# Kernel optimization log

Hardware: AMD Instinct MI355X
Metric: run time of the kernel (lower is better)

## Reference

```python
import jax, jax.numpy as jnp
import numpy as np

EPS = 1e-6
INF = 1e30  # stands in for 'no value' in the sparse C_bar lists of the torch code


def setup_inputs() -> dict:
    key = jax.random.key(0)
    M, N, D = 512, 256, 64
    kx, ky, kq = jax.random.split(key, 3)
    x = jax.random.normal(kx, (M, D), dtype=jnp.float32)
    y = jax.random.normal(ky, (N, D), dtype=jnp.float32)
    u = jax.random.uniform(kq, (N + 1, N), dtype=jnp.float32, minval=0.05, maxval=1.0)
    q = u / jnp.sum(u, axis=0, keepdims=True)  # column-stochastic jump probabilities
    return {"x": x, "y": y, "q": q}


def _pal_forward(x, y, q):
    M, N = x.shape[0], y.shape[0]
    dt = x.dtype

    # ---- compute_dists: pairwise L2 (p=2 norm), M x N ----
    diff = x[:, None, :] - y[None, :, :]
    dists = jnp.sqrt(jnp.sum(diff * diff, axis=2))

    # ---- compute_reachability: sequential accumulation over columns of q ----
    def reach_step(p, nb):
        return p + p[nb] * q[:, nb], None
    p0 = jnp.zeros(N + 1, dtype=dt).at[0].set(1.0)
    p, _ = jax.lax.scan(reach_step, p0, jnp.arange(N))
    p_back = p[:N][None, :] * q / (p[:, None] + EPS)  # (N+1, N)

    # ---- edge structure: ancestors n_bar < n with p_back > 0 (detached mask) ----
    tri = jnp.tril(jnp.ones((N, N), dtype=bool), k=-1)
    E = tri & (jax.lax.stop_gradient(p_back[:N]) > 0)   # (N, N): E[n, n_bar]
    w = jnp.where(E, p_back[:N], 0.0)                   # mixing weights

    ns = jnp.arange(1, N)

    def row_dp(d_row, base0, C_prev, Cbar_prev):
        """One row m of the lattice. C_prev: C[m-1] (N,), Cbar_prev: C_bar[m-1] (N,N).
        Returns C[m] (N,) and C_bar[m] (N,N) with INF at non-edge slots."""
        C0 = jnp.zeros(N, dtype=dt).at[0].set(d_row[0] + base0)

        def n_step(Ccur, n):
            # min over: C[m][n_bar] (insert y), C[m-1][n_bar] (match), C_bar[m-1][n][n_bar] (insert x)
            c_min = jnp.minimum(Ccur, jnp.minimum(C_prev, Cbar_prev[n]))  # (N,) over n_bar
            cbar = d_row[n] + c_min
            val = jnp.sum(jnp.where(E[n], w[n] * cbar, 0.0))
            return Ccur.at[n].set(val), jnp.where(E[n], cbar, INF)

        C_row, Cbar_rows = jax.lax.scan(n_step, C0, ns)
        Cbar = jnp.concatenate([jnp.full((1, N), INF, dt), Cbar_rows], axis=0)
        return C_row, Cbar

    # m = 0: no previous row -> previous-row candidates disabled via INF, C[0][0] = d[0,0]
    C_row0, Cbar0 = row_dp(dists[0], jnp.zeros((), dt), jnp.full(N, INF, dt), jnp.full((N, N), INF, dt))

    def m_step(carry, d_row):
        C_prev, Cbar_prev = carry
        C_row, Cbar = row_dp(d_row, C_prev[0], C_prev, Cbar_prev)  # C[m][0] = d[m,0] + C[m-1][0]
        return (C_row, Cbar), None

    (C_last, _), _ = jax.lax.scan(m_step, (C_row0, Cbar0), dists[1:])

    # expected cost of reaching END from each terminal n
    return jnp.sum(p_back[N] * C_last)


def reference(x, y, q):
    return _pal_forward(x, y, q)
```

## Files before the change

### kernel.cpp

```cpp
#include <hip/hip_runtime.h>

typedef float f4 __attribute__((ext_vector_type(4)));

#define Nn 256
#define Mm 512
#define Dd 64
#define EPSF 1e-6f
#define INFF 1e30f
#define BC 8
#define NCHUNK (Nn / BC)
#define R 16
#define NBLK 8
#define CW 4
#define SST (NBLK * CW)
#define SLOTS 4

#define OFF_D     0
#define OFF_QC    131072
#define OFF_P     (OFF_QC + 65792)
#define OFF_WT    (OFF_P + 260)
#define OFF_WS    (OFF_WT + 65536)
#define OFF_CBAR  (OFF_WS + 256)
#define OFF_CROW  (OFF_CBAR + 65536)
#define OFF_FLAG  (OFF_CROW + SST*Nn)

__device__ __forceinline__ int llc_load_int(const int* p) {
  int v;
  asm volatile("global_load_dword %0, %1, off sc0 sc1\n\ts_waitcnt vmcnt(0)"
               : "=v"(v) : "v"(p) : "memory");
  return v;
}
__device__ __forceinline__ void llc_store_int(int* p, int v) {
  asm volatile("global_store_dword %0, %1, off sc0 sc1" :: "v"(p), "v"(v) : "memory");
}
__device__ __forceinline__ void llc_load_cbar10(const float* b0, const float* cp,
                                                f4 c[8], f4& pl, f4& ph) {
  const float* b1 = b0 + 4 * Nn;
  asm volatile(
    "global_load_dwordx4 %0, %10, off sc0 sc1\n\t"
    "global_load_dwordx4 %1, %10, off offset:1024 sc0 sc1\n\t"
    "global_load_dwordx4 %2, %10, off offset:2048 sc0 sc1\n\t"
    "global_load_dwordx4 %3, %10, off offset:3072 sc0 sc1\n\t"
    "global_load_dwordx4 %4, %11, off sc0 sc1\n\t"
    "global_load_dwordx4 %5, %11, off offset:1024 sc0 sc1\n\t"
    "global_load_dwordx4 %6, %11, off offset:2048 sc0 sc1\n\t"
    "global_load_dwordx4 %7, %11, off offset:3072 sc0 sc1\n\t"
    "global_load_dwordx4 %8, %12, off sc0 sc1\n\t"
    "global_load_dwordx4 %9, %12, off offset:16 sc0 sc1\n\t"
    "s_waitcnt vmcnt(0)"
    : "=v"(c[0]), "=v"(c[1]), "=v"(c[2]), "=v"(c[3]),
      "=v"(c[4]), "=v"(c[5]), "=v"(c[6]), "=v"(c[7]),
      "=v"(pl), "=v"(ph)
    : "v"(b0), "v"(b1), "v"(cp)
    : "memory");
}
__device__ __forceinline__ void llc_store_cbar8(float* b0, const f4 c[8]) {
  float* b1 = b0 + 4 * Nn;
  asm volatile(
    "global_store_dwordx4 %8, %0, off sc0 sc1\n\t"
    "global_store_dwordx4 %8, %1, off offset:1024 sc0 sc1\n\t"
    "global_store_dwordx4 %8, %2, off offset:2048 sc0 sc1\n\t"
    "global_store_dwordx4 %8, %3, off offset:3072 sc0 sc1\n\t"
    "global_store_dwordx4 %9, %4, off sc0 sc1\n\t"
    "global_store_dwordx4 %9, %5, off offset:1024 sc0 sc1\n\t"
    "global_store_dwordx4 %9, %6, off offset:2048 sc0 sc1\n\t"
    "global_store_dwordx4 %9, %7, off offset:3072 sc0 sc1\n\t"
    "s_waitcnt vmcnt(0)"
    :: "v"(c[0]), "v"(c[1]), "v"(c[2]), "v"(c[3]),
       "v"(c[4]), "v"(c[5]), "v"(c[6]), "v"(c[7]),
       "v"(b0), "v"(b1)
    : "memory");
}
__device__ __forceinline__ float rdlane(float v, int l) {
  return __int_as_float(__builtin_amdgcn_readlane(__float_as_int(v), l));
}

__global__ __launch_bounds__(256) void k_pre(const float* __restrict__ x,
                                             const float* __restrict__ y,
                                             const float* __restrict__ q,
                                             float* __restrict__ ws) {
  const int b = blockIdx.x, t = threadIdx.x;
  if (b < Mm) {
    __shared__ float xs[Dd];
    if (t < Dd) xs[t] = x[b * Dd + t];
    __syncthreads();
    const float4* y4 = (const float4*)(y + t * Dd);
    float acc = 0.f;
#pragma unroll
    for (int k = 0; k < Dd / 4; k++) {
      float4 v = y4[k];
      float a0 = xs[4*k+0] - v.x, a1 = xs[4*k+1] - v.y;
      float a2 = xs[4*k+2] - v.z, a3 = xs[4*k+3] - v.w;
      acc += a0*a0 + a1*a1 + a2*a2 + a3*a3;
    }
    ws[OFF_D + b * Nn + t] = sqrtf(acc);
  } else if (b < Mm + 257) {
    const int j = b - Mm;
    ws[OFF_QC + t * 257 + j] = q[j * Nn + t];
  } else {
    ws[OFF_WS + t] = 0.f;
    if (t < NBLK * NCHUNK) ((int*)(ws + OFF_FLAG))[t] = 0;
  }
}

__global__ __launch_bounds__(256) void k_reach(const float* __restrict__ qc, float* __restrict__ p_out) {
  __shared__ float p[257];
  __shared__ float vsnap[64];
  __shared__ float qtile[64][65];
  int tid = threadIdx.x;
  p[tid] = (tid == 0) ? 1.f : 0.f;
  if (tid == 0) p[256] = 0.f;
  __syncthreads();
  for (int g = 0; g < 4; g++) {
    int g0 = g * 64;
    for (int z = 0; z < 16; z++) {
      int idx = tid + z * 256, k = idx >> 6, l = idx & 63;
      qtile[k][l] = qc[(g0 + k) * 257 + g0 + l];
    }
    __syncthreads();
    if (tid < 64) {
      float pv = p[g0 + tid];
      for (int k = 0; k < 64; k++) {
        float v = __shfl(pv, k, 64);
        if (tid == k) vsnap[k] = v;
        pv += v * qtile[k][tid];
      }
    }
    __syncthreads();
    float acc = p[tid];
    float acc2 = (tid == 0) ? p[256] : 0.f;
    for (int k = 0; k < 64; k++) {
      float v = vsnap[k];
      acc += v * qc[(g0 + k) * 257 + tid];
      if (tid == 0) acc2 += v * qc[(g0 + k) * 257 + 256];
    }
    __syncthreads();
    p[tid] = acc;
    if (tid == 0) p[256] = acc2;
    __syncthreads();
  }
  p_out[tid] = p[tid];
  if (tid == 0) p_out[256] = p[256];
}

__global__ __launch_bounds__(256) void k_wbuild(const float* __restrict__ qc, const float* __restrict__ p,
                                                float* __restrict__ wT, float* __restrict__ Wsum) {
  int t = blockIdx.x, n = threadIdx.x;
  float v = 0.f;
  if (t < n) v = p[t] * qc[t * 257 + n] / (p[n] + EPSF);
  wT[t * Nn + n] = v;
  if (v != 0.f) atomicAdd(&Wsum[n], v);
}

__global__ __launch_bounds__(320, 1) void k_main(const float* __restrict__ d,
                                                 const float* __restrict__ wT,
                                                 const float* __restrict__ Wsum,
                                                 float* __restrict__ cbarG,
                                                 float* __restrict__ crowG,
                                                 int* __restrict__ flags,
                                                 const float* __restrict__ q,
                                                 const float* __restrict__ p,
                                                 float* __restrict__ out) {
  __shared__ __align__(16) float sbuf[SLOTS][BC * Nn];
  __shared__ __align__(16) float stg[2][BC * Nn];
  __shared__ __align__(16) float stg_cr[2][8];
  __shared__ __align__(16) float crow_lds[CW][SLOTS][BC];
  __shared__ __align__(16) float crow_fin[Nn];

  const int tid  = threadIdx.x;
  const int wave = tid >> 6;
  const int lane = tid & 63;
  const int blk  = blockIdx.x;
  const int stage = blk * CW + wave;
  const int m0 = stage * R;

  f4 dl[R], S[R], Wt;
  if (wave < CW) {
#pragma unroll
    for (int r = 0; r < R; r++) {
      dl[r] = *(const f4*)(d + (m0 + r) * Nn + 4 * lane);
      S[r] = (f4){0.f, 0.f, 0.f, 0.f};
    }
    Wt = *(const f4*)(Wsum + 4 * lane);
  }

  if (wave == CW && blk > 0) {
    const int* fp = flags + (blk - 1) * NCHUNK;
    while (llc_load_int(fp) == 0) __builtin_amdgcn_s_sleep(1);
    f4 c0[BC], pl, ph;
    llc_load_cbar10(cbarG + 4 * lane, crowG + (blk - 1) * Nn, c0, pl, ph);
#pragma unroll
    for (int tt = 0; tt < BC; tt++) *(f4*)&stg[0][tt * Nn + 4 * lane] = c0[tt];
    if (lane == 0) { *(f4*)&stg_cr[0][0] = pl; *(f4*)&stg_cr[0][4] = ph; }
  }
  __syncthreads();

#pragma clang loop unroll(disable)
  for (int s = 0; s < NCHUNK + CW - 1; s++) {
    if (wave < CW) {
      const int j = s - wave;
      if (j >= 0 && j < NCHUNK) {
        f4 wv[BC];
#pragma unroll
        for (int tt = 0; tt < BC; tt++)
          wv[tt] = *(const f4*)(wT + (j * BC + tt) * Nn + 4 * lane);

        f4 c[BC], cpl, cph;
        float* lsl = &sbuf[j & (SLOTS - 1)][0] + 4 * lane;

        if (wave == 0) {
          if (blk > 0) {
#pragma unroll
            for (int tt = 0; tt < BC; tt++) c[tt] = *(const f4*)&stg[j & 1][tt * Nn + 4 * lane];
            cpl = *(const f4*)&stg_cr[j & 1][0];
            cph = *(const f4*)&stg_cr[j & 1][4];
          } else {
            cpl = (f4){INFF, INFF, INFF, INFF};
            cph = cpl;
#pragma unroll
            for (int tt = 0; tt < BC; tt++) c[tt] = cpl;
          }
        } else {
#pragma unroll
          for (int tt = 0; tt < BC; tt++) c[tt] = *(const f4*)(lsl + tt * Nn);
          const float* cr = &crow_lds[wave - 1][j & (SLOTS - 1)][0];
          cpl = *(const f4*)cr;
          cph = *(const f4*)(cr + 4);
        }

        f4 clast4;
        const bool isJ0 = (j == 0);
#pragma unroll
        for (int tt = 0; tt < BC; tt++) {
          const int owner = 2 * j + (tt >> 2);
          const int comp = tt & 3;
          const bool isT0 = isJ0 && (tt == 0);

          float up = (tt < 4) ? cpl[comp] : cph[comp];
          float prcMin = up;
          float prcVal = up;
          if (isT0 && stage == 0) prcVal = 0.f;
          float cml[R];
#pragma unroll
          for (int r = 0; r < R; r++) {
            float Cv;
            if (isT0) Cv = dl[r][0] + prcVal;
            else      Cv = fmaf(dl[r][comp], Wt[comp], S[r][comp]);
            cml[r] = fminf(Cv, prcMin);
            prcVal = Cv;
            prcMin = Cv;
          }
          float cmB[R];
#pragma unroll
          for (int r = 0; r < R; r++) cmB[r] = rdlane(cml[r], owner);
          float clastv = rdlane(prcVal, owner);
          if (lane == owner) clast4[comp] = clastv;

#pragma unroll
          for (int k = 0; k < 4; k++) {
            float w_ = wv[tt][k];
            if (w_ > 0.f) {
              float cbv = c[tt][k];
#pragma unroll
              for (int r = 0; r < R; r++) {
                float a = fminf(cmB[r], cbv);
                S[r][k] = fmaf(w_, a, S[r][k]);
                cbv = dl[r][k] + a;
              }
              c[tt][k] = cbv;
            }
          }
        }

        if (wave < CW - 1) {
#pragma unroll
          for (int tt = 0; tt < BC; tt++) *(f4*)(lsl + tt * Nn) = c[tt];
          if (lane == 2 * j || lane == 2 * j + 1)
            *(f4*)&crow_lds[wave][j & (SLOTS - 1)][(lane & 1) * 4] = clast4;
        } else if (blk < NBLK - 1) {
          if (lane == 2 * j || lane == 2 * j + 1) {
            float* cp = crowG + blk * Nn + j * BC + (lane & 1) * 4;
            asm volatile("global_store_dwordx4 %0, %1, off sc0 sc1" :: "v"(cp), "v"(clast4) : "memory");
          }
          llc_store_cbar8(cbarG + (size_t)j * BC * Nn + 4 * lane, c);
          if (lane == 0) llc_store_int(flags + blk * NCHUNK + j, 1);
        } else {
          if (lane == 2 * j || lane == 2 * j + 1)
            *(f4*)&crow_fin[j * BC + (lane & 1) * 4] = clast4;
        }
      }
    } else {
      const int jn = s + 1;
      if (blk > 0 && jn < NCHUNK) {
        const int* fp = flags + (blk - 1) * NCHUNK + jn;
        while (llc_load_int(fp) == 0) __builtin_amdgcn_s_sleep(1);
        f4 cn[BC], pl, ph;
        llc_load_cbar10(cbarG + (size_t)jn * BC * Nn + 4 * lane,
                        crowG + (blk - 1) * Nn + jn * BC, cn, pl, ph);
#pragma unroll
        for (int tt = 0; tt < BC; tt++) *(f4*)&stg[jn & 1][tt * Nn + 4 * lane] = cn[tt];
        if (lane == 0) { *(f4*)&stg_cr[jn & 1][0] = pl; *(f4*)&stg_cr[jn & 1][4] = ph; }
      }
    }
    __syncthreads();
  }

  if (blk == NBLK - 1) {
    if (tid < Nn) {
      float fw = p[tid] * q[Nn * Nn + tid] / (p[Nn] + EPSF);
      crow_fin[tid] *= fw;
    }
    __syncthreads();
    for (int sft = 128; sft > 0; sft >>= 1) {
      if (tid < sft) crow_fin[tid] += crow_fin[tid + sft];
      __syncthreads();
    }
    if (tid == 0) out[0] = crow_fin[0];
  }
}

extern "C" void kernel_launch(void* const* d_in, const int* in_sizes, int n_in,
                              void* d_out, int out_size, void* d_ws, size_t ws_size,
                              hipStream_t stream) {
  const float* x = (const float*)d_in[0];
  const float* y = (const float*)d_in[1];
  const float* q = (const float*)d_in[2];
  float* ws = (float*)d_ws;
  float* out = (float*)d_out;
  hipLaunchKernelGGL(k_pre,   dim3(Mm + 257 + 1), dim3(256), 0, stream, x, y, q, ws);
  hipLaunchKernelGGL(k_reach, dim3(1),   dim3(256), 0, stream, ws + OFF_QC, ws + OFF_P);
  hipLaunchKernelGGL(k_wbuild,dim3(Nn),  dim3(256), 0, stream, ws + OFF_QC, ws + OFF_P,
                     ws + OFF_WT, ws + OFF_WS);
  hipLaunchKernelGGL(k_main,  dim3(NBLK), dim3(320), 0, stream, ws + OFF_D, ws + OFF_WT,
                     ws + OFF_WS, ws + OFF_CBAR, ws + OFF_CROW, (int*)(ws + OFF_FLAG),
                     q, ws + OFF_P, out);
}
```

Before: 493.9 us.

## Offload inter-block cbar stores and prefetch to dedicated waves

Adds two prefetch waves that poll predecessor flags ahead and fill an 8-slot staging ring, plus a store wave that drains LDS-staged outputs to global memory and publishes flags with a delay. The last compute wave now writes its chunk to LDS instead of performing blocking LLC stores and waits. This aims to take global-memory latency off the compute waves' critical path, at the cost of more threads, more LDS, and later flag publication to the next block.

```diff
diff --git a/kernel.cpp b/kernel.cpp
--- a/kernel.cpp
+++ b/kernel.cpp
@@ -12,8 +12,10 @@
 #define R 16
 #define NBLK 8
 #define CW 4
+#define NPF 2
 #define SST (NBLK * CW)
 #define SLOTS 4
+#define SSLOT 8
 
 #define OFF_D     0
 #define OFF_QC    131072
@@ -54,7 +56,7 @@
     : "v"(b0), "v"(b1), "v"(cp)
     : "memory");
 }
-__device__ __forceinline__ void llc_store_cbar8(float* b0, const f4 c[8]) {
+__device__ __forceinline__ void llc_store_cbar8_nw(float* b0, const f4 c[8]) {
   float* b1 = b0 + 4 * Nn;
   asm volatile(
     "global_store_dwordx4 %8, %0, off sc0 sc1\n\t"
@@ -64,8 +66,7 @@
     "global_store_dwordx4 %9, %4, off sc0 sc1\n\t"
     "global_store_dwordx4 %9, %5, off offset:1024 sc0 sc1\n\t"
     "global_store_dwordx4 %9, %6, off offset:2048 sc0 sc1\n\t"
-    "global_store_dwordx4 %9, %7, off offset:3072 sc0 sc1\n\t"
-    "s_waitcnt vmcnt(0)"
+    "global_store_dwordx4 %9, %7, off offset:3072 sc0 sc1"
     :: "v"(c[0]), "v"(c[1]), "v"(c[2]), "v"(c[3]),
        "v"(c[4]), "v"(c[5]), "v"(c[6]), "v"(c[7]),
        "v"(b0), "v"(b1)
@@ -152,7 +153,7 @@
   if (v != 0.f) atomicAdd(&Wsum[n], v);
 }
 
-__global__ __launch_bounds__(320, 1) void k_main(const float* __restrict__ d,
+__global__ __launch_bounds__(448, 1) void k_main(const float* __restrict__ d,
                                                  const float* __restrict__ wT,
                                                  const float* __restrict__ Wsum,
                                                  float* __restrict__ cbarG,
@@ -162,8 +163,10 @@
                                                  const float* __restrict__ p,
                                                  float* __restrict__ out) {
   __shared__ __align__(16) float sbuf[SLOTS][BC * Nn];
-  __shared__ __align__(16) float stg[2][BC * Nn];
-  __shared__ __align__(16) float stg_cr[2][8];
+  __shared__ __align__(16) float stg[SSLOT][BC * Nn];
+  __shared__ __align__(16) float stg_cr[SSLOT][8];
+  __shared__ __align__(16) float ostg[2][BC * Nn];
+  __shared__ __align__(16) float ostg_cr[2][8];
   __shared__ __align__(16) float crow_lds[CW][SLOTS][BC];
   __shared__ __align__(16) float crow_fin[Nn];
 
@@ -184,14 +187,21 @@
     Wt = *(const f4*)(Wsum + 4 * lane);
   }
 
-  if (wave == CW && blk > 0) {
-    const int* fp = flags + (blk - 1) * NCHUNK;
-    while (llc_load_int(fp) == 0) __builtin_amdgcn_s_sleep(1);
-    f4 c0[BC], pl, ph;
-    llc_load_cbar10(cbarG + 4 * lane, crowG + (blk - 1) * Nn, c0, pl, ph);
-#pragma unroll
-    for (int tt = 0; tt < BC; tt++) *(f4*)&stg[0][tt * Nn + 4 * lane] = c0[tt];
-    if (lane == 0) { *(f4*)&stg_cr[0][0] = pl; *(f4*)&stg_cr[0][4] = ph; }
+  int jn = NCHUNK, pend = 0;
+  if (wave >= CW && wave < CW + NPF) {
+    const int pf = wave - CW;
+    if (blk > 0) {
+      jn = pf;
+      const int* fp = flags + (blk - 1) * NCHUNK + jn;
+      while (llc_load_int(fp) == 0) __builtin_amdgcn_s_sleep(1);
+      f4 cn[BC], pl, ph;
+      llc_load_cbar10(cbarG + (size_t)jn * BC * Nn + 4 * lane,
+                      crowG + (blk - 1) * Nn + jn * BC, cn, pl, ph);
+#pragma unroll
+      for (int tt = 0; tt < BC; tt++) *(f4*)&stg[jn][tt * Nn + 4 * lane] = cn[tt];
+      if (lane == 0) { *(f4*)&stg_cr[jn][0] = pl; *(f4*)&stg_cr[jn][4] = ph; }
+      jn += NPF;
+    }
   }
   __syncthreads();
 
@@ -211,9 +221,9 @@
         if (wave == 0) {
           if (blk > 0) {
 #pragma unroll
-            for (int tt = 0; tt < BC; tt++) c[tt] = *(const f4*)&stg[j & 1][tt * Nn + 4 * lane];
-            cpl = *(const f4*)&stg_cr[j & 1][0];
-            cph = *(const f4*)&stg_cr[j & 1][4];
+            for (int tt = 0; tt < BC; tt++) c[tt] = *(const f4*)&stg[j & (SSLOT - 1)][tt * Nn + 4 * lane];
+            cpl = *(const f4*)&stg_cr[j & (SSLOT - 1)][0];
+            cph = *(const f4*)&stg_cr[j & (SSLOT - 1)][4];
           } else {
             cpl = (f4){INFF, INFF, INFF, INFF};
             cph = cpl;
@@ -278,31 +288,72 @@
           if (lane == 2 * j || lane == 2 * j + 1)
             *(f4*)&crow_lds[wave][j & (SLOTS - 1)][(lane & 1) * 4] = clast4;
         } else if (blk < NBLK - 1) {
-          if (lane == 2 * j || lane == 2 * j + 1) {
-            float* cp = crowG + blk * Nn + j * BC + (lane & 1) * 4;
-            asm volatile("global_store_dwordx4 %0, %1, off sc0 sc1" :: "v"(cp), "v"(clast4) : "memory");
-          }
-          llc_store_cbar8(cbarG + (size_t)j * BC * Nn + 4 * lane, c);
-          if (lane == 0) llc_store_int(flags + blk * NCHUNK + j, 1);
+#pragma unroll
+          for (int tt = 0; tt < BC; tt++) *(f4*)&ostg[j & 1][tt * Nn + 4 * lane] = c[tt];
+          if (lane == 2 * j || lane == 2 * j + 1)
+            *(f4*)&ostg_cr[j & 1][(lane & 1) * 4] = clast4;
         } else {
           if (lane == 2 * j || lane == 2 * j + 1)
             *(f4*)&crow_fin[j * BC + (lane & 1) * 4] = clast4;
         }
       }
+    } else if (wave < CW + NPF) {
+      if (blk > 0 && jn < NCHUNK) {
+        if (pend) {
+          f4 cn[BC], pl, ph;
+          llc_load_cbar10(cbarG + (size_t)jn * BC * Nn + 4 * lane,
+                          crowG + (blk - 1) * Nn + jn * BC, cn, pl, ph);
+#pragma unroll
+          for (int tt = 0; tt < BC; tt++) *(f4*)&stg[jn & (SSLOT - 1)][tt * Nn + 4 * lane] = cn[tt];
+          if (lane == 0) {
+            *(f4*)&stg_cr[jn & (SSLOT - 1)][0] = pl;
+            *(f4*)&stg_cr[jn & (SSLOT - 1)][4] = ph;
+          }
+          jn += NPF; pend = 0;
+        } else if (s >= jn - 4) {
+          const int* fp = flags + (blk - 1) * NCHUNK + jn;
+          if (s >= jn - 2) {
+            while (llc_load_int(fp) == 0) __builtin_amdgcn_s_sleep(1);
+            pend = 1;
+          } else if (llc_load_int(fp) != 0) pend = 1;
+        }
+      }
     } else {
-      const int jn = s + 1;
-      if (blk > 0 && jn < NCHUNK) {
-        const int* fp = flags + (blk - 1) * NCHUNK + jn;
-        while (llc_load_int(fp) == 0) __builtin_amdgcn_s_sleep(1);
-        f4 cn[BC], pl, ph;
-        llc_load_cbar10(cbarG + (size_t)jn * BC * Nn + 4 * lane,
-                        crowG + (blk - 1) * Nn + jn * BC, cn, pl, ph);
-#pragma unroll
-        for (int tt = 0; tt < BC; tt++) *(f4*)&stg[jn & 1][tt * Nn + 4 * lane] = cn[tt];
-        if (lane == 0) { *(f4*)&stg_cr[jn & 1][0] = pl; *(f4*)&stg_cr[jn & 1][4] = ph; }
+      if (blk < NBLK - 1) {
+        asm volatile("s_waitcnt vmcnt(0)" ::: "memory");
+        const int c_pub = s - 5;
+        if (c_pub >= 0 && lane == 0) llc_store_int(flags + blk * NCHUNK + c_pub, 1);
+        const int c_st = s - 4;
+        if (c_st >= 0 && c_st < NCHUNK) {
+          f4 co[BC];
+#pragma unroll
+          for (int tt = 0; tt < BC; tt++) co[tt] = *(const f4*)&ostg[c_st & 1][tt * Nn + 4 * lane];
+          llc_store_cbar8_nw(cbarG + (size_t)c_st * BC * Nn + 4 * lane, co);
+          if (lane < 2) {
+            f4 cr = *(const f4*)&ostg_cr[c_st & 1][lane * 4];
+            float* cp = crowG + blk * Nn + c_st * BC + lane * 4;
+            asm volatile("global_store_dwordx4 %0, %1, off sc0 sc1" :: "v"(cp), "v"(cr) : "memory");
+          }
+        }
       }
     }
     __syncthreads();
+  }
+
+  if (wave == CW + NPF && blk < NBLK - 1) {
+    asm volatile("s_waitcnt vmcnt(0)" ::: "memory");
+    if (lane == 0) llc_store_int(flags + blk * NCHUNK + (NCHUNK - 2), 1);
+    f4 co[BC];
+#pragma unroll
+    for (int tt = 0; tt < BC; tt++) co[tt] = *(const f4*)&ostg[(NCHUNK - 1) & 1][tt * Nn + 4 * lane];
+    llc_store_cbar8_nw(cbarG + (size_t)(NCHUNK - 1) * BC * Nn + 4 * lane, co);
+    if (lane < 2) {
+      f4 cr = *(const f4*)&ostg_cr[(NCHUNK - 1) & 1][lane * 4];
+      float* cp = crowG + blk * Nn + (NCHUNK - 1) * BC + lane * 4;
+      asm volatile("global_store_dwordx4 %0, %1, off sc0 sc1" :: "v"(cp), "v"(cr) : "memory");
+    }
+    asm volatile("s_waitcnt vmcnt(0)" ::: "memory");
+    if (lane == 0) llc_store_int(flags + blk * NCHUNK + (NCHUNK - 1), 1);
   }
 
   if (blk == NBLK - 1) {
@@ -331,7 +382,7 @@
   hipLaunchKernelGGL(k_reach, dim3(1),   dim3(256), 0, stream, ws + OFF_QC, ws + OFF_P);
   hipLaunchKernelGGL(k_wbuild,dim3(Nn),  dim3(256), 0, stream, ws + OFF_QC, ws + OFF_P,
                      ws + OFF_WT, ws + OFF_WS);
-  hipLaunchKernelGGL(k_main,  dim3(NBLK), dim3(320), 0, stream, ws + OFF_D, ws + OFF_WT,
+  hipLaunchKernelGGL(k_main,  dim3(NBLK), dim3(448), 0, stream, ws + OFF_D, ws + OFF_WT,
                      ws + OFF_WS, ws + OFF_CBAR, ws + OFF_CROW, (int*)(ws + OFF_FLAG),
                      q, ws + OFF_P, out);
 }
```

New measurement: 546.5 us. 1.11x slower.
